# Kernel optimization log

Hardware: AMD Instinct MI355X
Metric: run time of the kernel (lower is better)

Reference implementation:

```python
import jax, jax.numpy as jnp
import numpy as np

M = 8192          # flattened tokens (batch*seq)
IN_FEATURES = 4096
OUT_FEATURES = 4096


def setup_inputs() -> dict:
    key = jax.random.key(0)
    k1, k2, k3 = jax.random.split(key, 3)
    # int8-valued activations and weights, stored as int32 (values in [-128, 127])
    x = jax.random.randint(k1, (M, IN_FEATURES), -128, 128, dtype=jnp.int32)
    int_weight = jax.random.randint(k2, (OUT_FEATURES, IN_FEATURES), -128, 127, dtype=jnp.int32)
    bias = (jax.random.normal(k3, (OUT_FEATURES,), dtype=jnp.float32) * 0.02).astype(jnp.float16)
    return {"x": x, "int_weight": int_weight, "bias": bias}


def reference(x, int_weight, bias):
    # x.to(torch.int8); quik int8Matmul: int8 GEMM with int32 accumulation, out = x @ W^T
    x_i8 = x.astype(jnp.int8)
    w_i8 = int_weight.astype(jnp.int8)
    acc = jax.lax.dot_general(
        x_i8, w_i8,
        dimension_numbers=(((1,), (1,)), ((), ())),  # [M, K] x [N, K] -> [M, N]
        preferred_element_type=jnp.int32,
    )
    # .to(torch.float16) then bias add (fused epilogue target)
    return acc.astype(jnp.float16) + bias
```

## Files before the change

kernel.cpp:

```cpp
#include <hip/hip_runtime.h>

#define MDIM 8192
#define NDIM 4096
#define KDIM 4096
#define BM 256
#define BN 256
#define BK 128

typedef int v4i __attribute__((ext_vector_type(4)));
typedef int v16i __attribute__((ext_vector_type(16)));

__device__ __forceinline__ unsigned pack4(int x, int y, int z, int w) {
    return (unsigned)(x & 0xff) | ((unsigned)(y & 0xff) << 8) |
           ((unsigned)(z & 0xff) << 16) | ((unsigned)w << 24);
}

__global__ __launch_bounds__(256) void pack_tiled(const int* __restrict__ x,
                                                  const int* __restrict__ w,
                                                  uint4* __restrict__ xp,
                                                  uint4* __restrict__ wp) {
    __shared__ unsigned lds32[256 * 33];
    const int wg  = blockIdx.x;
    const int tid = threadIdx.x;
    const int kq   = tid & 31;
    const int rsub = tid >> 5;

    const int* src;
    uint4* dst;
    if (wg < 1024) {
        const int mtile = wg >> 5, kiter = wg & 31;
        src = x + (size_t)(mtile * 256) * KDIM + kiter * 128;
        dst = xp + (size_t)(mtile * 32 + kiter) * 2048;
    } else {
        const int ntile = (wg - 1024) >> 5, kiter = wg & 31;
        src = w + (size_t)(ntile * 256) * KDIM + kiter * 128;
        dst = wp + (size_t)(ntile * 32 + kiter) * 2048;
    }
#pragma unroll
    for (int it = 0; it < 32; ++it) {
        const int row = it * 8 + rsub;
        int4 v = *(const int4*)(src + (size_t)row * KDIM + kq * 4);
        lds32[row * 33 + kq] = pack4(v.x, v.y, v.z, v.w);
    }
    __syncthreads();
#pragma unroll
    for (int it = 0; it < 8; ++it) {
        const int g = it * 256 + tid;
        const int kb = g >> 8, row = g & 255;
        const unsigned* p = &lds32[row * 33 + kb * 4];
        uint4 o;
        o.x = p[0]; o.y = p[1]; o.z = p[2]; o.w = p[3];
        dst[g] = o;
    }
}

__global__ __launch_bounds__(512, 2) void gemm_i8_pipe(const char* __restrict__ Ap,
                                                       const char* __restrict__ Bp,
                                                       const _Float16* __restrict__ bias,
                                                       _Float16* __restrict__ out) {
    __shared__ __align__(16) char lds[65536];

    const int tid  = threadIdx.x;
    const int lane = tid & 63;
    const int wave = tid >> 6;
    const int wr   = wave >> 2;
    const int wcn  = wave & 3;
    const int l31  = lane & 31;
    const int kg   = lane >> 5;

    const int lid = blockIdx.y * 16 + blockIdx.x;
    const int xc  = lid & 7, ii = lid >> 3;
    const int bx  = (xc & 3) * 4 + (ii & 3);
    const int by  = (xc >> 2) * 16 + (ii >> 2);
    const int bm0 = by * BM;
    const int bn0 = bx * BN;

    const char* apan = Ap + (size_t)by * (BM * KDIM) + tid * 16;
    const char* bpan = Bp + (size_t)bx * (BN * KDIM);

    int aoff[4], boffG[2];
#pragma unroll
    for (int mt = 0; mt < 4; ++mt)
        aoff[mt] = (wr * 128 + mt * 32 + l31) * 16 + kg * 4096;
#pragma unroll
    for (int nt = 0; nt < 2; ++nt)
        boffG[nt] = (wcn * 64 + nt * 32 + l31) * 16 + kg * 4096;

    v16i acc[4][2];
#pragma unroll
    for (int mt = 0; mt < 4; ++mt)
#pragma unroll
        for (int nt = 0; nt < 2; ++nt)
#pragma unroll
            for (int i = 0; i < 16; ++i) acc[mt][nt][i] = 0;

    v4i afP[4], afQ[4];
    v4i bfE[2][2], bfL[2][2];

    auto stageA = [&](int nb) {
#pragma unroll
        for (int c2 = 0; c2 < 4; ++c2)
            __builtin_amdgcn_global_load_lds(
                (__attribute__((address_space(1))) const void*)(apan + c2 * 8192),
                (__attribute__((address_space(3))) void*)(lds + nb + c2 * 8192 + tid * 16),
                16, 0, 0);
    };
    auto loadB2 = [&](v4i (&d)[2][2], int ksb) {
#pragma unroll
        for (int nt = 0; nt < 2; ++nt)
#pragma unroll
            for (int k = 0; k < 2; ++k)
                d[nt][k] = *(const v4i*)(bpan + boffG[nt] + (ksb + k) * 8192);
    };
    auto readA = [&](v4i (&d)[4], int base, int ks) {
#pragma unroll
        for (int mt = 0; mt < 4; ++mt)
            d[mt] = *(const v4i*)(lds + base + ks * 8192 + aoff[mt]);
    };
    auto cl = [&](const v4i (&a)[4], const v4i (&b)[2][2], int k) {
        __builtin_amdgcn_s_setprio(1);
#pragma unroll
        for (int mt = 0; mt < 4; ++mt)
#pragma unroll
            for (int nt = 0; nt < 2; ++nt)
                acc[mt][nt] = __builtin_amdgcn_mfma_i32_32x32x32_i8(
                    a[mt], b[nt][k], acc[mt][nt], 0, 0, 0);
        __builtin_amdgcn_s_setprio(0);
    };

#define SB0 __builtin_amdgcn_sched_barrier(0)
#define TOPBAR do { asm volatile("s_waitcnt vmcnt(0)" ::: "memory"); \
                    __builtin_amdgcn_s_barrier(); } while (0)

    stageA(0);
    TOPBAR; SB0;
    loadB2(bfE, 0);
    stageA(32768);
    apan += BM * BK;
    SB0;
    loadB2(bfL, 2);
    readA(afP, 0, 0);
    readA(afQ, 0, 1);
    SB0;
    cl(afP, bfE, 0);
    SB0;
    readA(afP, 0, 2);
    SB0;
    cl(afQ, bfE, 1);
    SB0;
    readA(afQ, 0, 3);
    bpan += BN * BK;
    SB0;

#pragma unroll 1
    for (int t = 1; t < 32; ++t) {
        const int cur = (t & 1) ? 32768 : 0;
        TOPBAR; SB0;
        loadB2(bfE, 0);
        stageA(cur ^ 32768);
        apan += BM * BK;
        SB0;
        cl(afP, bfL, 0);
        SB0;
        readA(afP, cur, 0);
        SB0;
        cl(afQ, bfL, 1);
        SB0;
        readA(afQ, cur, 1);
        loadB2(bfL, 2);
        SB0;
        cl(afP, bfE, 0);
        SB0;
        readA(afP, cur, 2);
        SB0;
        cl(afQ, bfE, 1);
        SB0;
        readA(afQ, cur, 3);
        bpan += BN * BK;
        SB0;
    }
    cl(afP, bfL, 0);
    cl(afQ, bfL, 1);

#undef SB0
#undef TOPBAR

    const _Float16 bv0 = bias[bn0 + wcn * 64 + l31];
    const _Float16 bv1 = bias[bn0 + wcn * 64 + 32 + l31];
#pragma unroll
    for (int mt = 0; mt < 4; ++mt) {
#pragma unroll
        for (int nt = 0; nt < 2; ++nt) {
            const int gcol = bn0 + wcn * 64 + nt * 32 + l31;
            const _Float16 bb = nt ? bv1 : bv0;
#pragma unroll
            for (int r = 0; r < 16; ++r) {
                const int rit  = (r & 3) + 8 * (r >> 2) + 4 * kg;
                const int grow = bm0 + wr * 128 + mt * 32 + rit;
                _Float16 h = (_Float16)(float)acc[mt][nt][r] + bb;
                out[(size_t)grow * NDIM + gcol] = h;
            }
        }
    }
}

__global__ __launch_bounds__(256, 2) void gemm_i8_fb(const int* __restrict__ A32,
                                                     const int* __restrict__ B32,
                                                     const _Float16* __restrict__ bias,
                                                     _Float16* __restrict__ out) {
    __shared__ char lds[32768];
    const int tid  = threadIdx.x;
    const int lane = tid & 63;
    const int wave = tid >> 6;
    const int bm0 = blockIdx.y * 256;
    const int bn0 = blockIdx.x * 128;
    const int wr  = wave >> 1;
    const int wc  = wave & 1;
    const int l31 = lane & 31;
    const int kg  = lane >> 5;

    int abase[4];
#pragma unroll
    for (int mt = 0; mt < 4; ++mt)
        abase[mt] = kg * 4096 + (wr * 128 + mt * 32 + l31) * 16;

    v16i acc[4][2];
#pragma unroll
    for (int mt = 0; mt < 4; ++mt)
#pragma unroll
        for (int nt = 0; nt < 2; ++nt)
#pragma unroll
            for (int i = 0; i < 16; ++i) acc[mt][nt][i] = 0;

    int aoffs[8];
#pragma unroll
    for (int r = 0; r < 8; ++r) {
        const int c = r * 4 + wave;
        aoffs[r] = (bm0 + (c & 3) * 64 + lane) * KDIM + (c >> 2) * 16;
    }
    for (int k0 = 0; k0 < KDIM; k0 += 128) {
        v4i bfx[2][4];
#pragma unroll
        for (int r = 0; r < 8; ++r) {
            const int c = r * 4 + wave;
            const int4* s = (const int4*)(A32 + (size_t)aoffs[r]);
            int4 v0 = s[0], v1 = s[1], v2 = s[2], v3 = s[3];
            uint4 pk;
            pk.x = pack4(v0.x, v0.y, v0.z, v0.w);
            pk.y = pack4(v1.x, v1.y, v1.z, v1.w);
            pk.z = pack4(v2.x, v2.y, v2.z, v2.w);
            pk.w = pack4(v3.x, v3.y, v3.z, v3.w);
            *(uint4*)(lds + c * 1024 + lane * 16) = pk;
            aoffs[r] += 128;
        }
#pragma unroll
        for (int nt = 0; nt < 2; ++nt)
#pragma unroll
            for (int ks = 0; ks < 4; ++ks) {
                const int* s = B32 + (size_t)(bn0 + wc * 64 + nt * 32 + l31) * KDIM
                               + k0 + (2 * ks + kg) * 16;
                int4 v0 = ((const int4*)s)[0], v1 = ((const int4*)s)[1];
                int4 v2 = ((const int4*)s)[2], v3 = ((const int4*)s)[3];
                bfx[nt][ks][0] = (int)pack4(v0.x, v0.y, v0.z, v0.w);
                bfx[nt][ks][1] = (int)pack4(v1.x, v1.y, v1.z, v1.w);
                bfx[nt][ks][2] = (int)pack4(v2.x, v2.y, v2.z, v2.w);
                bfx[nt][ks][3] = (int)pack4(v3.x, v3.y, v3.z, v3.w);
            }
        __syncthreads();
#pragma unroll
        for (int ks = 0; ks < 4; ++ks) {
            v4i afr[4];
#pragma unroll
            for (int mt = 0; mt < 4; ++mt)
                afr[mt] = *(const v4i*)(lds + abase[mt] + ks * 8192);
#pragma unroll
            for (int mt = 0; mt < 4; ++mt)
#pragma unroll
                for (int nt = 0; nt < 2; ++nt)
                    acc[mt][nt] = __builtin_amdgcn_mfma_i32_32x32x32_i8(
                        afr[mt], bfx[nt][ks], acc[mt][nt], 0, 0, 0);
        }
        __syncthreads();
    }

    const _Float16 bv0 = bias[bn0 + wc * 64 + l31];
    const _Float16 bv1 = bias[bn0 + wc * 64 + 32 + l31];
#pragma unroll
    for (int mt = 0; mt < 4; ++mt) {
#pragma unroll
        for (int nt = 0; nt < 2; ++nt) {
            const int gcol = bn0 + wc * 64 + nt * 32 + l31;
            const _Float16 bb = nt ? bv1 : bv0;
#pragma unroll
            for (int r = 0; r < 16; ++r) {
                const int rit  = (r & 3) + 8 * (r >> 2) + 4 * kg;
                const int grow = bm0 + wr * 128 + mt * 32 + rit;
                _Float16 h = (_Float16)(float)acc[mt][nt][r] + bb;
                out[(size_t)grow * NDIM + gcol] = h;
            }
        }
    }
}

extern "C" void kernel_launch(void* const* d_in, const int* in_sizes, int n_in,
                              void* d_out, int out_size, void* d_ws, size_t ws_size,
                              hipStream_t stream) {
    const int* x = (const int*)d_in[0];
    const int* w = (const int*)d_in[1];
    const _Float16* bias = (const _Float16*)d_in[2];
    _Float16* out = (_Float16*)d_out;

    const size_t xbytes = (size_t)MDIM * KDIM;
    const size_t wbytes = (size_t)NDIM * KDIM;

    if (ws_size >= xbytes + wbytes) {
        char* xp = (char*)d_ws;
        char* wp = xp + xbytes;
        pack_tiled<<<1536, 256, 0, stream>>>(x, w, (uint4*)xp, (uint4*)wp);
        gemm_i8_pipe<<<dim3(NDIM / BN, MDIM / BM), 512, 0, stream>>>(
            (const char*)xp, (const char*)wp, bias, out);
    } else {
        gemm_i8_fb<<<dim3(NDIM / 128, MDIM / 256), 256, 0, stream>>>(
            x, w, bias, out);
    }
}
```

Measured before the change: 390.3 us.

## Stage B tiles through double-buffered LDS alongside A instead of direct global loads

```diff
diff --git a/kernel.cpp b/kernel.cpp
--- a/kernel.cpp
+++ b/kernel.cpp
@@ -54,11 +54,11 @@
     }
 }
 
-__global__ __launch_bounds__(512, 2) void gemm_i8_pipe(const char* __restrict__ Ap,
+__global__ __launch_bounds__(512, 2) void gemm_i8_hold(const char* __restrict__ Ap,
                                                        const char* __restrict__ Bp,
                                                        const _Float16* __restrict__ bias,
                                                        _Float16* __restrict__ out) {
-    __shared__ __align__(16) char lds[65536];
+    __shared__ __align__(16) char lds[131072];
 
     const int tid  = threadIdx.x;
     const int lane = tid & 63;
@@ -76,15 +76,15 @@
     const int bn0 = bx * BN;
 
     const char* apan = Ap + (size_t)by * (BM * KDIM) + tid * 16;
-    const char* bpan = Bp + (size_t)bx * (BN * KDIM);
-
-    int aoff[4], boffG[2];
+    const char* bpan = Bp + (size_t)bx * (BN * KDIM) + tid * 16;
+
+    int aoff[4], boff[2];
 #pragma unroll
     for (int mt = 0; mt < 4; ++mt)
         aoff[mt] = (wr * 128 + mt * 32 + l31) * 16 + kg * 4096;
 #pragma unroll
     for (int nt = 0; nt < 2; ++nt)
-        boffG[nt] = (wcn * 64 + nt * 32 + l31) * 16 + kg * 4096;
+        boff[nt] = (wcn * 64 + nt * 32 + l31) * 16 + kg * 4096;
 
     v16i acc[4][2];
 #pragma unroll
@@ -105,17 +105,25 @@
                 (__attribute__((address_space(3))) void*)(lds + nb + c2 * 8192 + tid * 16),
                 16, 0, 0);
     };
-    auto loadB2 = [&](v4i (&d)[2][2], int ksb) {
-#pragma unroll
-        for (int nt = 0; nt < 2; ++nt)
-#pragma unroll
-            for (int k = 0; k < 2; ++k)
-                d[nt][k] = *(const v4i*)(bpan + boffG[nt] + (ksb + k) * 8192);
+    auto stageB = [&](int nb) {
+#pragma unroll
+        for (int c2 = 0; c2 < 4; ++c2)
+            __builtin_amdgcn_global_load_lds(
+                (__attribute__((address_space(1))) const void*)(bpan + c2 * 8192),
+                (__attribute__((address_space(3))) void*)(lds + nb + 32768 + c2 * 8192 + tid * 16),
+                16, 0, 0);
     };
     auto readA = [&](v4i (&d)[4], int base, int ks) {
 #pragma unroll
         for (int mt = 0; mt < 4; ++mt)
             d[mt] = *(const v4i*)(lds + base + ks * 8192 + aoff[mt]);
+    };
+    auto readB2 = [&](v4i (&d)[2][2], int base, int ksb) {
+#pragma unroll
+        for (int nt = 0; nt < 2; ++nt)
+#pragma unroll
+            for (int k = 0; k < 2; ++k)
+                d[nt][k] = *(const v4i*)(lds + base + 32768 + (ksb + k) * 8192 + boff[nt]);
     };
     auto cl = [&](const v4i (&a)[4], const v4i (&b)[2][2], int k) {
         __builtin_amdgcn_s_setprio(1);
@@ -132,15 +140,17 @@
 #define TOPBAR do { asm volatile("s_waitcnt vmcnt(0)" ::: "memory"); \
                     __builtin_amdgcn_s_barrier(); } while (0)
 
-    stageA(0);
+    stageA(0); stageB(0);
+    apan += BM * BK; bpan += BN * BK;
     TOPBAR; SB0;
-    loadB2(bfE, 0);
-    stageA(32768);
-    apan += BM * BK;
-    SB0;
-    loadB2(bfL, 2);
+    readB2(bfE, 0, 0);
     readA(afP, 0, 0);
+    SB0;
+    stageA(65536); stageB(65536);
+    apan += BM * BK; bpan += BN * BK;
+    SB0;
     readA(afQ, 0, 1);
+    readB2(bfL, 0, 2);
     SB0;
     cl(afP, bfE, 0);
     SB0;
@@ -149,16 +159,13 @@
     cl(afQ, bfE, 1);
     SB0;
     readA(afQ, 0, 3);
-    bpan += BN * BK;
     SB0;
 
 #pragma unroll 1
     for (int t = 1; t < 32; ++t) {
-        const int cur = (t & 1) ? 32768 : 0;
+        const int cur = (t & 1) ? 65536 : 0;
         TOPBAR; SB0;
-        loadB2(bfE, 0);
-        stageA(cur ^ 32768);
-        apan += BM * BK;
+        readB2(bfE, cur, 0);
         SB0;
         cl(afP, bfL, 0);
         SB0;
@@ -166,8 +173,13 @@
         SB0;
         cl(afQ, bfL, 1);
         SB0;
+        if (t < 31) {
+            stageA(cur ^ 65536);
+            stageB(cur ^ 65536);
+            apan += BM * BK; bpan += BN * BK;
+        }
         readA(afQ, cur, 1);
-        loadB2(bfL, 2);
+        readB2(bfL, cur, 2);
         SB0;
         cl(afP, bfE, 0);
         SB0;
@@ -176,7 +188,6 @@
         cl(afQ, bfE, 1);
         SB0;
         readA(afQ, cur, 3);
-        bpan += BN * BK;
         SB0;
     }
     cl(afP, bfL, 0);
@@ -317,7 +328,7 @@
         char* xp = (char*)d_ws;
         char* wp = xp + xbytes;
         pack_tiled<<<1536, 256, 0, stream>>>(x, w, (uint4*)xp, (uint4*)wp);
-        gemm_i8_pipe<<<dim3(NDIM / BN, MDIM / BM), 512, 0, stream>>>(
+        gemm_i8_hold<<<dim3(NDIM / BN, MDIM / BM), 512, 0, stream>>>(
             (const char*)xp, (const char*)wp, bias, out);
     } else {
         gemm_i8_fb<<<dim3(NDIM / 128, MDIM / 256), 256, 0, stream>>>(
```

Measured after the change: 377.5 us. -3.3%, faster.

## Prefetch full B k-tile into registers one iteration ahead

Applied to the files above, without the earlier changes.

```diff
diff --git a/kernel.cpp b/kernel.cpp
--- a/kernel.cpp
+++ b/kernel.cpp
@@ -54,7 +54,7 @@
     }
 }
 
-__global__ __launch_bounds__(512, 2) void gemm_i8_pipe(const char* __restrict__ Ap,
+__global__ __launch_bounds__(512, 2) void gemm_i8_breg(const char* __restrict__ Ap,
                                                        const char* __restrict__ Bp,
                                                        const _Float16* __restrict__ bias,
                                                        _Float16* __restrict__ out) {
@@ -95,7 +95,7 @@
             for (int i = 0; i < 16; ++i) acc[mt][nt][i] = 0;
 
     v4i afP[4], afQ[4];
-    v4i bfE[2][2], bfL[2][2];
+    v4i bfX[2][4], bfY[2][4];
 
     auto stageA = [&](int nb) {
 #pragma unroll
@@ -105,19 +105,19 @@
                 (__attribute__((address_space(3))) void*)(lds + nb + c2 * 8192 + tid * 16),
                 16, 0, 0);
     };
-    auto loadB2 = [&](v4i (&d)[2][2], int ksb) {
+    auto loadB = [&](v4i (&d)[2][4]) {
 #pragma unroll
         for (int nt = 0; nt < 2; ++nt)
 #pragma unroll
-            for (int k = 0; k < 2; ++k)
-                d[nt][k] = *(const v4i*)(bpan + boffG[nt] + (ksb + k) * 8192);
+            for (int ks = 0; ks < 4; ++ks)
+                d[nt][ks] = *(const v4i*)(bpan + boffG[nt] + ks * 8192);
     };
     auto readA = [&](v4i (&d)[4], int base, int ks) {
 #pragma unroll
         for (int mt = 0; mt < 4; ++mt)
             d[mt] = *(const v4i*)(lds + base + ks * 8192 + aoff[mt]);
     };
-    auto cl = [&](const v4i (&a)[4], const v4i (&b)[2][2], int k) {
+    auto cl = [&](const v4i (&a)[4], const v4i (&b)[2][4], int k) {
         __builtin_amdgcn_s_setprio(1);
 #pragma unroll
         for (int mt = 0; mt < 4; ++mt)
@@ -132,55 +132,40 @@
 #define TOPBAR do { asm volatile("s_waitcnt vmcnt(0)" ::: "memory"); \
                     __builtin_amdgcn_s_barrier(); } while (0)
 
+    auto body = [&](int cur, const v4i (&bf)[2][4], int nxt, v4i (&bfn)[2][4],
+                    bool stg) {
+        TOPBAR; SB0;
+        readA(afP, cur, 0);
+        readA(afQ, cur, 1);
+        SB0;
+        if (stg) {
+            stageA(nxt);
+            loadB(bfn);
+            apan += BM * BK;
+            bpan += BN * BK;
+        }
+        SB0;
+        cl(afP, bf, 0); SB0;
+        readA(afP, cur, 2); SB0;
+        cl(afQ, bf, 1); SB0;
+        readA(afQ, cur, 3); SB0;
+        cl(afP, bf, 2); SB0;
+        cl(afQ, bf, 3);
+    };
+
     stageA(0);
-    TOPBAR; SB0;
-    loadB2(bfE, 0);
-    stageA(32768);
+    loadB(bfX);
     apan += BM * BK;
-    SB0;
-    loadB2(bfL, 2);
-    readA(afP, 0, 0);
-    readA(afQ, 0, 1);
-    SB0;
-    cl(afP, bfE, 0);
-    SB0;
-    readA(afP, 0, 2);
-    SB0;
-    cl(afQ, bfE, 1);
-    SB0;
-    readA(afQ, 0, 3);
     bpan += BN * BK;
-    SB0;
+
+    body(0, bfX, 32768, bfY, true);
 
 #pragma unroll 1
-    for (int t = 1; t < 32; ++t) {
-        const int cur = (t & 1) ? 32768 : 0;
-        TOPBAR; SB0;
-        loadB2(bfE, 0);
-        stageA(cur ^ 32768);
-        apan += BM * BK;
-        SB0;
-        cl(afP, bfL, 0);
-        SB0;
-        readA(afP, cur, 0);
-        SB0;
-        cl(afQ, bfL, 1);
-        SB0;
-        readA(afQ, cur, 1);
-        loadB2(bfL, 2);
-        SB0;
-        cl(afP, bfE, 0);
-        SB0;
-        readA(afP, cur, 2);
-        SB0;
-        cl(afQ, bfE, 1);
-        SB0;
-        readA(afQ, cur, 3);
-        bpan += BN * BK;
-        SB0;
-    }
-    cl(afP, bfL, 0);
-    cl(afQ, bfL, 1);
+    for (int p = 0; p < 15; ++p) {
+        body(32768, bfY, 0, bfX, true);
+        body(0, bfX, 32768, bfY, true);
+    }
+    body(32768, bfY, 0, bfX, false);
 
 #undef SB0
 #undef TOPBAR
@@ -317,7 +302,7 @@
         char* xp = (char*)d_ws;
         char* wp = xp + xbytes;
         pack_tiled<<<1536, 256, 0, stream>>>(x, w, (uint4*)xp, (uint4*)wp);
-        gemm_i8_pipe<<<dim3(NDIM / BN, MDIM / BM), 512, 0, stream>>>(
+        gemm_i8_breg<<<dim3(NDIM / BN, MDIM / BM), 512, 0, stream>>>(
             (const char*)xp, (const char*)wp, bias, out);
     } else {
         gemm_i8_fb<<<dim3(NDIM / 128, MDIM / 256), 256, 0, stream>>>(
```

Result: no change. 386.0 us (-1.1%).
